# Kernel tuning notes

Measured on AMD Instinct MI355X. Metric: run time of the kernel, lower is better.

Reference implementation:

```python
import jax, jax.numpy as jnp
import numpy as np

EMBED_DIM = 1024
NUM_HEADS = 16
HEAD_DIM = EMBED_DIM // NUM_HEADS
B, L = 4, 2048


def _xavier(key, out_dim, in_dim):
    limit = jnp.sqrt(6.0 / (in_dim + out_dim))
    return jax.random.uniform(key, (out_dim, in_dim), jnp.float32, -limit, limit)


def setup_inputs() -> dict:
    key = jax.random.key(0)
    kx, kq, kk, kv, ko = jax.random.split(key, 5)
    return {
        "x": jax.random.normal(kx, (B, L, EMBED_DIM), jnp.float32),
        "Wq": _xavier(kq, EMBED_DIM, EMBED_DIM), "bq": jnp.zeros((EMBED_DIM,), jnp.float32),
        "Wk": _xavier(kk, EMBED_DIM, EMBED_DIM), "bk": jnp.zeros((EMBED_DIM,), jnp.float32),
        "Wv": _xavier(kv, EMBED_DIM, EMBED_DIM), "bv": jnp.zeros((EMBED_DIM,), jnp.float32),
        "Wo": _xavier(ko, EMBED_DIM, EMBED_DIM), "bo": jnp.zeros((EMBED_DIM,), jnp.float32),
    }


def reference(x, Wq, bq, Wk, bk, Wv, bv, Wo, bo):
    bs, l, e = x.shape
    h, hd = NUM_HEADS, HEAD_DIM
    # torch Linear: y = x @ W.T + b
    q = (x @ Wq.T + bq).reshape(bs, l, h, hd).transpose(0, 2, 1, 3)  # [b,h,l,hd]
    k = (x @ Wk.T + bk).reshape(bs, l, h, hd).transpose(0, 2, 1, 3)
    v = (x @ Wv.T + bv).reshape(bs, l, h, hd).transpose(0, 2, 1, 3)
    scale = 1.0 / jnp.sqrt(jnp.asarray(hd, x.dtype))
    scores = jnp.einsum("bhqd,bhkd->bhqk", q, k) * scale  # [b,h,l,l]
    attn = jax.nn.softmax(scores, axis=-1)
    out = jnp.einsum("bhqk,bhkd->bhqd", attn, v)  # [b,h,l,hd]
    out = out.transpose(0, 2, 1, 3).reshape(bs, l, e)
    return out @ Wo.T + bo
```

## Files before the change

kernel.cpp:

```cpp
#include <hip/hip_runtime.h>
#include <hip/hip_bf16.h>
#include <stdint.h>

#define NB 4
#define NL 2048
#define NE 1024
#define NH 16
#define ND 64
#define NM (NB*NL)

typedef float f32x4 __attribute__((ext_vector_type(4)));
typedef float f32x16 __attribute__((ext_vector_type(16)));
typedef short s16x8 __attribute__((ext_vector_type(8)));
typedef unsigned int u32x4 __attribute__((ext_vector_type(4)));

__device__ __forceinline__ unsigned short f2b(float f) {
  uint32_t u = __float_as_uint(f);
  u += 0x7fffu + ((u >> 16) & 1u);
  return (unsigned short)(u >> 16);
}

__device__ __forceinline__ uint32_t pk2(float a, float b) {
  __hip_bfloat162 h = __float22bfloat162_rn(make_float2(a, b));
  union { __hip_bfloat162 h; uint32_t u; } c; c.h = h; return c.u;
}

__device__ __forceinline__ void gload16(const void* g, void* l) {
  __builtin_amdgcn_global_load_lds((const __attribute__((address_space(1))) void*)g,
                                   (__attribute__((address_space(3))) void*)l, 16, 0, 0);
}

__global__ void cvt_kernel(const float* __restrict__ in, unsigned short* __restrict__ out, int n8) {
  int stride = gridDim.x * blockDim.x;
  for (int i = blockIdx.x * blockDim.x + threadIdx.x; i < n8; i += stride) {
    const float4* p = (const float4*)in + (size_t)i * 2;
    float4 a = p[0], b = p[1];
    uint4 r;
    r.x = pk2(a.x, a.y); r.y = pk2(a.z, a.w);
    r.z = pk2(b.x, b.y); r.w = pk2(b.z, b.w);
    *((uint4*)out + i) = r;
  }
}

__global__ void cvt4_kernel(const float* __restrict__ w0, const float* __restrict__ w1,
                            const float* __restrict__ w2, const float* __restrict__ w3,
                            unsigned short* __restrict__ o0, unsigned short* __restrict__ o1,
                            unsigned short* __restrict__ o2, unsigned short* __restrict__ o3,
                            int n8) {
  const int y = blockIdx.y;
  const float* in = (y == 0) ? w0 : (y == 1) ? w1 : (y == 2) ? w2 : w3;
  unsigned short* out = (y == 0) ? o0 : (y == 1) ? o1 : (y == 2) ? o2 : o3;
  int stride = gridDim.x * blockDim.x;
  for (int i = blockIdx.x * blockDim.x + threadIdx.x; i < n8; i += stride) {
    const float4* p = (const float4*)in + (size_t)i * 2;
    float4 a = p[0], b = p[1];
    uint4 r;
    r.x = pk2(a.x, a.y); r.y = pk2(a.z, a.w);
    r.z = pk2(b.x, b.y); r.w = pk2(b.z, b.w);
    *((uint4*)out + i) = r;
  }
}

template<int MODE>
__launch_bounds__(256, 2)
__global__ void gemm_bt(const unsigned short* __restrict__ A,
                        const unsigned short* __restrict__ W0,
                        const unsigned short* __restrict__ W1,
                        const unsigned short* __restrict__ W2,
                        const float* __restrict__ b0,
                        const float* __restrict__ b1,
                        const float* __restrict__ b2,
                        unsigned short* __restrict__ O0,
                        unsigned short* __restrict__ O1,
                        unsigned short* __restrict__ O2,
                        float* __restrict__ fout)
{
  __shared__ alignas(16) char smem[32768];
  char* sA = smem;
  char* sB = smem + 16384;

  const int tid = threadIdx.x;
  const int lane = tid & 63;
  const int wid = tid >> 6;
  const int bx = blockIdx.x, by = blockIdx.y;
  const int m0 = by * 128;

  int which = 0;
  const unsigned short* Wsel;
  const float* bias;
  int n0;
  if (MODE == 0) {
    which = bx >> 3;
    Wsel = (which == 0) ? W0 : ((which == 1) ? W1 : W2);
    bias = (which == 0) ? b0 : ((which == 1) ? b1 : b2);
    n0 = (bx & 7) * 128;
  } else {
    Wsel = W0; bias = b0; n0 = bx * 128;
  }

  const int wr = (wid >> 1) * 64;
  const int wc = (wid & 1) * 64;
  int aaddr[4], baddr[4];
#pragma unroll
  for (int m = 0; m < 4; ++m) {
    int ra = wr + m * 16 + (lane & 15);
    aaddr[m] = ra * 128 + (((lane >> 4) * 16) ^ ((ra & 7) << 4));
    int rb = wc + m * 16 + (lane & 15);
    baddr[m] = rb * 128 + (((lane >> 4) * 16) ^ ((rb & 7) << 4));
  }

  f32x4 acc[4][4] = {};
  const int c0 = wid * 64 + lane;

  for (int kt = 0; kt < 16; ++kt) {
    const int k0 = kt * 64;
#pragma unroll
    for (int it = 0; it < 4; ++it) {
      int c = it * 256 + c0;
      int row = c >> 3;
      int sb = ((((c & 7) << 4)) ^ ((row & 7) << 4)) >> 1;
      gload16(A    + (size_t)(m0 + row) * NE + k0 + sb, sA + it * 4096 + wid * 1024);
      gload16(Wsel + (size_t)(n0 + row) * NE + k0 + sb, sB + it * 4096 + wid * 1024);
    }
    __syncthreads();
#pragma unroll
    for (int kk = 0; kk < 2; ++kk) {
      s16x8 af[4], bf[4];
#pragma unroll
      for (int m = 0; m < 4; ++m) af[m] = *(const s16x8*)(sA + (aaddr[m] ^ (kk << 6)));
#pragma unroll
      for (int n = 0; n < 4; ++n) bf[n] = *(const s16x8*)(sB + (baddr[n] ^ (kk << 6)));
#pragma unroll
      for (int m = 0; m < 4; ++m)
#pragma unroll
        for (int n = 0; n < 4; ++n)
          acc[m][n] = __builtin_amdgcn_mfma_f32_16x16x32_bf16(af[m], bf[n], acc[m][n], 0, 0, 0);
    }
    __syncthreads();
  }

  const float qsc = (MODE == 0 && ((bx >> 3) == 0)) ? 0.18033688011112042f : 1.0f;
#pragma unroll
  for (int m = 0; m < 4; ++m) {
    const int row0 = m0 + wr + m * 16 + ((lane >> 4) << 2);
#pragma unroll
    for (int n = 0; n < 4; ++n) {
      const int col = n0 + wc + n * 16 + (lane & 15);
      const float bv = bias[col];
      if (MODE == 1) {
#pragma unroll
        for (int r = 0; r < 4; ++r)
          fout[(size_t)(row0 + r) * NE + col] = acc[m][n][r] + bv;
      } else {
        const int b = row0 >> 11;
        const int l = row0 & 2047;
        const int h = col >> 6;
        const int d = col & 63;
        if (which < 2) {
          unsigned short* dst = (which == 0) ? O0 : O1;
#pragma unroll
          for (int r = 0; r < 4; ++r)
            dst[((size_t)(b * NH + h) * NL + (l + r)) * ND + d] = f2b((acc[m][n][r] + bv) * qsc);
        } else {
          uint2 w;
          w.x = pk2(acc[m][n][0] + bv, acc[m][n][1] + bv);
          w.y = pk2(acc[m][n][2] + bv, acc[m][n][3] + bv);
          *(uint2*)(O2 + ((size_t)(b * NH + h) * ND + d) * NL + l) = w;
        }
      }
    }
  }
}

__launch_bounds__(256, 4)
__global__ void attn_kernel(const unsigned short* __restrict__ Q,
                            const unsigned short* __restrict__ K,
                            const unsigned short* __restrict__ Vt,
                            unsigned short* __restrict__ AO)
{
  __shared__ alignas(16) char smem[32768];

  const int tid = threadIdx.x;
  const int lane = tid & 63;
  const int wid = tid >> 6;
  const int ql = lane & 31;
  const int hh = lane >> 5;
  const int qt = blockIdx.x;
  const int bh = blockIdx.y;
  const int b = bh >> 4;
  const int h = bh & 15;
  const size_t base = (size_t)bh * NL * ND;
  const int q0 = qt * 128 + wid * 32;

  s16x8 qf[4];
#pragma unroll
  for (int ks = 0; ks < 4; ++ks)
    qf[ks] = *(const s16x8*)(Q + base + (size_t)(q0 + ql) * ND + ks * 16 + hh * 8);

  int fa[2][4];
#pragma unroll
  for (int t = 0; t < 2; ++t)
#pragma unroll
    for (int ks = 0; ks < 4; ++ks) {
      int r = t * 32 + ql;
      fa[t][ks] = r * 128 + ((ks * 32 + hh * 16) ^ ((r & 7) << 4));
    }

  f32x16 o0 = {}, o1 = {};
  float rm = -1e30f, rl = 0.f;

#define STAGE(T, BUF)                                                          \
  do {                                                                         \
    const int kv0_ = (T) * 64;                                                 \
    char* sKb_ = smem + (BUF) * 8192;                                          \
    char* sVb_ = smem + 16384 + (BUF) * 8192;                                  \
    _Pragma("unroll")                                                          \
    for (int it = 0; it < 2; ++it) {                                           \
      int c = it * 256 + wid * 64 + lane;                                      \
      int row = c >> 3;                                                        \
      int sb = (((c & 7) << 4) ^ ((row & 7) << 4)) >> 1;                       \
      gload16(K  + base + (size_t)(kv0_ + row) * ND + sb,                      \
              sKb_ + it * 4096 + wid * 1024);                                  \
      gload16(Vt + base + (size_t)row * NL + kv0_ + sb,                        \
              sVb_ + it * 4096 + wid * 1024);                                  \
    }                                                                          \
  } while (0)

  STAGE(0, 0);
  __syncthreads();

  for (int t = 0; t < 32; ++t) {
    const int cur = t & 1;
    if (t < 31) STAGE(t + 1, cur ^ 1);
    const char* sKb = smem + cur * 8192;
    const char* sVb = smem + 16384 + cur * 8192;

    f32x16 s0 = {}, s1 = {};
    __builtin_amdgcn_s_setprio(1);
#pragma unroll
    for (int ks = 0; ks < 4; ++ks) {
      s16x8 kf0 = *(const s16x8*)(sKb + fa[0][ks]);
      s16x8 kf1 = *(const s16x8*)(sKb + fa[1][ks]);
      s0 = __builtin_amdgcn_mfma_f32_32x32x16_bf16(kf0, qf[ks], s0, 0, 0, 0);
      s1 = __builtin_amdgcn_mfma_f32_32x32x16_bf16(kf1, qf[ks], s1, 0, 0, 0);
    }
    __builtin_amdgcn_s_setprio(0);

    float q0m = fmaxf(fmaxf(s0[0], s0[1]), fmaxf(s0[2], s0[3]));
    float q1m = fmaxf(fmaxf(s0[4], s0[5]), fmaxf(s0[6], s0[7]));
    float q2m = fmaxf(fmaxf(s0[8], s0[9]), fmaxf(s0[10], s0[11]));
    float q3m = fmaxf(fmaxf(s0[12], s0[13]), fmaxf(s0[14], s0[15]));
    float q4m = fmaxf(fmaxf(s1[0], s1[1]), fmaxf(s1[2], s1[3]));
    float q5m = fmaxf(fmaxf(s1[4], s1[5]), fmaxf(s1[6], s1[7]));
    float q6m = fmaxf(fmaxf(s1[8], s1[9]), fmaxf(s1[10], s1[11]));
    float q7m = fmaxf(fmaxf(s1[12], s1[13]), fmaxf(s1[14], s1[15]));
    float pm = fmaxf(fmaxf(fmaxf(q0m, q1m), fmaxf(q2m, q3m)),
                     fmaxf(fmaxf(q4m, q5m), fmaxf(q6m, q7m)));
    pm = fmaxf(pm, __shfl_xor(pm, 32));

    float mn = rm;
    if (!__all(pm - mn <= 8.0f)) {
      mn = fmaxf(mn, pm);
      float al = __builtin_amdgcn_exp2f(rm - mn);
      rl *= al;
      o0 = o0 * al;
      o1 = o1 * al;
      rm = mn;
    }

    uint32_t w0[8], w1[8];
    float ts0 = 0.f, ts1 = 0.f, ts2 = 0.f, ts3 = 0.f;
#pragma unroll
    for (int i = 0; i < 8; ++i) {
      float e0 = __builtin_amdgcn_exp2f(s0[2 * i]     - mn);
      float e1 = __builtin_amdgcn_exp2f(s0[2 * i + 1] - mn);
      float e2 = __builtin_amdgcn_exp2f(s1[2 * i]     - mn);
      float e3 = __builtin_amdgcn_exp2f(s1[2 * i + 1] - mn);
      ts0 += e0; ts1 += e1; ts2 += e2; ts3 += e3;
      w0[i] = pk2(e0, e1);
      w1[i] = pk2(e2, e3);
    }
    float ts = (ts0 + ts1) + (ts2 + ts3);
    ts += __shfl_xor(ts, 32);
    rl += ts;

    s16x8 pfr[4];
#pragma unroll
    for (int tt = 0; tt < 2; ++tt) {
      const uint32_t* w = tt ? w1 : w0;
      u32x4 lo, hi;
#pragma unroll
      for (int aa = 0; aa < 2; ++aa) {
        uint32_t v  = hh ? w[aa] : w[aa + 2];
        uint32_t sv = (uint32_t)__shfl_xor((int)v, 32);
        lo[aa]     = hh ? sv        : w[aa];
        lo[aa + 2] = hh ? w[aa + 2] : sv;
      }
#pragma unroll
      for (int aa = 0; aa < 2; ++aa) {
        uint32_t v  = hh ? w[aa + 4] : w[aa + 6];
        uint32_t sv = (uint32_t)__shfl_xor((int)v, 32);
        hi[aa]     = hh ? sv        : w[aa + 4];
        hi[aa + 2] = hh ? w[aa + 6] : sv;
      }
      pfr[2 * tt]     = __builtin_bit_cast(s16x8, lo);
      pfr[2 * tt + 1] = __builtin_bit_cast(s16x8, hi);
    }

    __builtin_amdgcn_s_setprio(1);
#pragma unroll
    for (int ks = 0; ks < 4; ++ks) {
      s16x8 vf0 = *(const s16x8*)(sVb + fa[0][ks]);
      s16x8 vf1 = *(const s16x8*)(sVb + fa[1][ks]);
      o0 = __builtin_amdgcn_mfma_f32_32x32x16_bf16(vf0, pfr[ks], o0, 0, 0, 0);
      o1 = __builtin_amdgcn_mfma_f32_32x32x16_bf16(vf1, pfr[ks], o1, 0, 0, 0);
    }
    __builtin_amdgcn_s_setprio(0);
    __syncthreads();
  }
#undef STAGE

  const float inv = 1.0f / rl;
  const size_t orow = (size_t)(b * NL + q0 + ql) * NE + h * 64;
#pragma unroll
  for (int q4 = 0; q4 < 4; ++q4) {
    uint2 wv;
    wv.x = pk2(o0[4 * q4] * inv, o0[4 * q4 + 1] * inv);
    wv.y = pk2(o0[4 * q4 + 2] * inv, o0[4 * q4 + 3] * inv);
    *(uint2*)(AO + orow + 4 * hh + 8 * q4) = wv;
  }
#pragma unroll
  for (int q4 = 0; q4 < 4; ++q4) {
    uint2 wv;
    wv.x = pk2(o1[4 * q4] * inv, o1[4 * q4 + 1] * inv);
    wv.y = pk2(o1[4 * q4 + 2] * inv, o1[4 * q4 + 3] * inv);
    *(uint2*)(AO + orow + 32 + 4 * hh + 8 * q4) = wv;
  }
}

extern "C" void kernel_launch(void* const* d_in, const int* in_sizes, int n_in,
                              void* d_out, int out_size, void* d_ws, size_t ws_size,
                              hipStream_t stream) {
  const float* x  = (const float*)d_in[0];
  const float* Wq = (const float*)d_in[1];
  const float* bq = (const float*)d_in[2];
  const float* Wk = (const float*)d_in[3];
  const float* bk = (const float*)d_in[4];
  const float* Wv = (const float*)d_in[5];
  const float* bv = (const float*)d_in[6];
  const float* Wo = (const float*)d_in[7];
  const float* bo = (const float*)d_in[8];
  float* out = (float*)d_out;
  char* ws = (char*)d_ws;

  unsigned short* xb  = (unsigned short*)(ws);
  unsigned short* AOw = (unsigned short*)(ws);
  unsigned short* wqb = (unsigned short*)(ws + (16u << 20));
  unsigned short* wkb = (unsigned short*)(ws + (18u << 20));
  unsigned short* wvb = (unsigned short*)(ws + (20u << 20));
  unsigned short* wob = (unsigned short*)(ws + (22u << 20));
  unsigned short* Qw  = (unsigned short*)(ws + (24u << 20));
  unsigned short* Kw  = (unsigned short*)(ws + (40u << 20));
  unsigned short* Vtw = (unsigned short*)(ws + (56u << 20));
  (void)in_sizes; (void)n_in; (void)out_size; (void)ws_size;

  cvt_kernel<<<1024, 256, 0, stream>>>(x, xb, (NM * NE) / 8);
  cvt4_kernel<<<dim3(128, 4), 256, 0, stream>>>(Wq, Wk, Wv, Wo,
                                                wqb, wkb, wvb, wob, (NE * NE) / 8);

  gemm_bt<0><<<dim3(24, 64), 256, 0, stream>>>(xb, wqb, wkb, wvb, bq, bk, bv,
                                               Qw, Kw, Vtw, nullptr);
  attn_kernel<<<dim3(16, 64), 256, 0, stream>>>(Qw, Kw, Vtw, AOw);
  gemm_bt<1><<<dim3(8, 64), 256, 0, stream>>>(AOw, wob, nullptr, nullptr, bo,
                                              nullptr, nullptr,
                                              nullptr, nullptr, nullptr, out);
}
```

Before: 298.5 us.

## Merge conversion kernels, precompute attention load addresses, drop GEMM launch bounds

The x and four weight fp32-to-bf16 conversions are merged into one grid-stride kernel, saving a launch and the gap between two small kernels. The attention kernel's K/V staging now precomputes per-thread global pointers and LDS offsets once, so each stage only adds a tile offset instead of recomputing swizzled addresses. The __launch_bounds__(256,2) hint on the GEMM is removed, which changes the compiler's register budget and may alter occupancy or spilling.

```diff
diff --git a/kernel.cpp b/kernel.cpp
--- a/kernel.cpp
+++ b/kernel.cpp
@@ -30,39 +30,35 @@
                                    (__attribute__((address_space(3))) void*)l, 16, 0, 0);
 }
 
-__global__ void cvt_kernel(const float* __restrict__ in, unsigned short* __restrict__ out, int n8) {
+__global__ void cvt_all_kernel(const float* __restrict__ x,
+                               const float* __restrict__ w0, const float* __restrict__ w1,
+                               const float* __restrict__ w2, const float* __restrict__ w3,
+                               unsigned short* __restrict__ xb,
+                               unsigned short* __restrict__ o0, unsigned short* __restrict__ o1,
+                               unsigned short* __restrict__ o2, unsigned short* __restrict__ o3) {
+  const int NX = (NM * NE) / 8;
+  const int NW = (NE * NE) / 8;
   int stride = gridDim.x * blockDim.x;
-  for (int i = blockIdx.x * blockDim.x + threadIdx.x; i < n8; i += stride) {
-    const float4* p = (const float4*)in + (size_t)i * 2;
+  for (int i = blockIdx.x * blockDim.x + threadIdx.x; i < NX + 4 * NW; i += stride) {
+    const float* in; unsigned short* out; int off;
+    if (i < NX) { in = x; out = xb; off = i; }
+    else {
+      int j = i - NX;
+      int s = j >> 17;
+      off = j & (NW - 1);
+      in  = (s == 0) ? w0 : (s == 1) ? w1 : (s == 2) ? w2 : w3;
+      out = (s == 0) ? o0 : (s == 1) ? o1 : (s == 2) ? o2 : o3;
+    }
+    const float4* p = (const float4*)in + (size_t)off * 2;
     float4 a = p[0], b = p[1];
     uint4 r;
     r.x = pk2(a.x, a.y); r.y = pk2(a.z, a.w);
     r.z = pk2(b.x, b.y); r.w = pk2(b.z, b.w);
-    *((uint4*)out + i) = r;
-  }
-}
-
-__global__ void cvt4_kernel(const float* __restrict__ w0, const float* __restrict__ w1,
-                            const float* __restrict__ w2, const float* __restrict__ w3,
-                            unsigned short* __restrict__ o0, unsigned short* __restrict__ o1,
-                            unsigned short* __restrict__ o2, unsigned short* __restrict__ o3,
-                            int n8) {
-  const int y = blockIdx.y;
-  const float* in = (y == 0) ? w0 : (y == 1) ? w1 : (y == 2) ? w2 : w3;
-  unsigned short* out = (y == 0) ? o0 : (y == 1) ? o1 : (y == 2) ? o2 : o3;
-  int stride = gridDim.x * blockDim.x;
-  for (int i = blockIdx.x * blockDim.x + threadIdx.x; i < n8; i += stride) {
-    const float4* p = (const float4*)in + (size_t)i * 2;
-    float4 a = p[0], b = p[1];
-    uint4 r;
-    r.x = pk2(a.x, a.y); r.y = pk2(a.z, a.w);
-    r.z = pk2(b.x, b.y); r.w = pk2(b.z, b.w);
-    *((uint4*)out + i) = r;
+    *((uint4*)out + off) = r;
   }
 }
 
 template<int MODE>
-__launch_bounds__(256, 2)
 __global__ void gemm_bt(const unsigned short* __restrict__ A,
                         const unsigned short* __restrict__ W0,
                         const unsigned short* __restrict__ W1,
@@ -206,23 +202,28 @@
       fa[t][ks] = r * 128 + ((ks * 32 + hh * 16) ^ ((r & 7) << 4));
     }
 
+  const unsigned short* gK[2];
+  const unsigned short* gV[2];
+  int ldsOff[2];
+#pragma unroll
+  for (int it = 0; it < 2; ++it) {
+    int c = it * 256 + wid * 64 + lane;
+    int row = c >> 3;
+    int sb = (((c & 7) << 4) ^ ((row & 7) << 4)) >> 1;
+    gK[it] = K  + base + (size_t)row * ND + sb;
+    gV[it] = Vt + base + (size_t)row * NL + sb;
+    ldsOff[it] = it * 4096 + wid * 1024;
+  }
+
   f32x16 o0 = {}, o1 = {};
   float rm = -1e30f, rl = 0.f;
 
 #define STAGE(T, BUF)                                                          \
   do {                                                                         \
-    const int kv0_ = (T) * 64;                                                 \
-    char* sKb_ = smem + (BUF) * 8192;                                          \
-    char* sVb_ = smem + 16384 + (BUF) * 8192;                                  \
     _Pragma("unroll")                                                          \
     for (int it = 0; it < 2; ++it) {                                           \
-      int c = it * 256 + wid * 64 + lane;                                      \
-      int row = c >> 3;                                                        \
-      int sb = (((c & 7) << 4) ^ ((row & 7) << 4)) >> 1;                       \
-      gload16(K  + base + (size_t)(kv0_ + row) * ND + sb,                      \
-              sKb_ + it * 4096 + wid * 1024);                                  \
-      gload16(Vt + base + (size_t)row * NL + kv0_ + sb,                        \
-              sVb_ + it * 4096 + wid * 1024);                                  \
+      gload16(gK[it] + (T) * 4096, smem + (BUF) * 8192 + ldsOff[it]);          \
+      gload16(gV[it] + (T) * 64,   smem + 16384 + (BUF) * 8192 + ldsOff[it]);  \
     }                                                                          \
   } while (0)
 
@@ -364,9 +365,8 @@
   unsigned short* Vtw = (unsigned short*)(ws + (56u << 20));
   (void)in_sizes; (void)n_in; (void)out_size; (void)ws_size;
 
-  cvt_kernel<<<1024, 256, 0, stream>>>(x, xb, (NM * NE) / 8);
-  cvt4_kernel<<<dim3(128, 4), 256, 0, stream>>>(Wq, Wk, Wv, Wo,
-                                                wqb, wkb, wvb, wob, (NE * NE) / 8);
+  cvt_all_kernel<<<2048, 256, 0, stream>>>(x, Wq, Wk, Wv, Wo,
+                                           xb, wqb, wkb, wvb, wob);
 
   gemm_bt<0><<<dim3(24, 64), 256, 0, stream>>>(xb, wqb, wkb, wvb, bq, bk, bv,
                                                Qw, Kw, Vtw, nullptr);
```

Result: no change. 303.7 us (+1.7%).
